# Kernel optimization log

Measured on AMD Instinct MI355X. Metric: run time of the kernel, lower is better.

## Reference

```python
import jax, jax.numpy as jnp
import numpy as np

N_USERS = 20000
N_ITEMS = 30000
N = N_USERS + N_ITEMS          # total nodes
D = 64                          # embedding_dim
EXTRA = 1152                    # 768 metadata + 384 review
E = 500000                      # full-graph edges
NC = 100                        # clusters
HEADS = 2                       # per-layer GATConv heads
CG_HEADS = 4                    # GlobalGATOverClusters hard-codes heads=4
L = 2                           # num_layers
ED = 2                          # edge_dim


def _gat(x, ei, ea, lin, a_src, a_dst, lin_e, a_edge, bias, heads, nnodes):
    """PyG GATConv: add self loops (edge_attr fill='mean'), concat=False -> head mean."""
    C = a_src.shape[-1]
    loop = jnp.arange(nnodes)
    src = jnp.concatenate([ei[0], loop])
    dst = jnp.concatenate([ei[1], loop])
    ea_full = jnp.concatenate([ea, jnp.broadcast_to(ea.mean(0), (nnodes, ea.shape[1]))], 0)
    xh = (x @ lin).reshape(nnodes, heads, C)            # [N,H,C]
    asrc = (xh * a_src).sum(-1)                         # [N,H]
    adst = (xh * a_dst).sum(-1)
    eh = (ea_full @ lin_e).reshape(-1, heads, C)        # [Etot,H,C]
    ae = (eh * a_edge).sum(-1)                          # [Etot,H]
    al = jax.nn.leaky_relu(asrc[src] + adst[dst] + ae, 0.2)
    amax = jax.ops.segment_max(al, dst, num_segments=nnodes)
    ex = jnp.exp(al - amax[dst])
    s = jax.ops.segment_sum(ex, dst, num_segments=nnodes)
    w = ex / (s[dst] + 1e-16)
    out = jax.ops.segment_sum(xh[src] * w[..., None], dst, num_segments=nnodes)
    return out.mean(1) + bias


def _graph_norm(x, weight, bias, mean_scale, eps=1e-5):
    mean = x.mean(0)
    out = x - mean_scale * mean
    var = (out * out).mean(0)
    return weight * out * jax.lax.rsqrt(var + eps) + bias


def _forward(product_extra_features, user_emb, item_emb, fus_w1, fus_b1, fus_w2, fus_b2,
             full_edge_attr, gcn_w, gcn_b,
             cg_lin, cg_att_src, cg_att_dst, cg_lin_edge, cg_att_edge, cg_bias, cluster_edge_attr,
             gat_lin, gat_att_src, gat_att_dst, gat_lin_edge, gat_att_edge, gat_bias,
             gn_weight, gn_bias, gn_mean_scale,
             full_edge_index, cluster_assignment, cluster_edge_index):
    # fusion MLP on item side (dropout is identity at inference)
    h = jnp.maximum(jnp.concatenate([item_emb, product_extra_features], -1) @ fus_w1 + fus_b1, 0.0)
    enriched_items = h @ fus_w2 + fus_b2
    X = jnp.concatenate([user_emb, enriched_items], 0)  # [N, D]

    # per-cluster GCN == one GCN over intra-cluster edges + self loops;
    # nodes in clusters with zero intra edges keep original features
    ei0, ei1 = full_edge_index[0], full_edge_index[1]
    intra = cluster_assignment[ei0] == cluster_assignment[ei1]
    loop = jnp.arange(N)
    row = jnp.concatenate([ei0, loop])
    col = jnp.concatenate([ei1, loop])
    ew = jnp.concatenate([intra.astype(X.dtype), jnp.ones((N,), X.dtype)])
    deg = jax.ops.segment_sum(ew, col, num_segments=N)
    dinv = jnp.where(deg > 0, jax.lax.rsqrt(deg), 0.0)
    norm = dinv[row] * ew * dinv[col]
    xw = X @ gcn_w
    gcn_out = jax.ops.segment_sum(xw[row] * norm[:, None], col, num_segments=N) + gcn_b
    cl_has_edge = jax.ops.segment_sum(intra.astype(jnp.int32), cluster_assignment[ei0], num_segments=NC) > 0
    Xc = jnp.where(cl_has_edge[cluster_assignment][:, None], gcn_out, X)

    # mean pool per cluster
    cnt = jax.ops.segment_sum(jnp.ones((N,), X.dtype), cluster_assignment, num_segments=NC)
    pooled = jax.ops.segment_sum(Xc, cluster_assignment, num_segments=NC) / jnp.maximum(cnt, 1.0)[:, None]

    # global GAT over clusters (inter-cluster multigraph, precomputed)
    cl_upd = _gat(pooled, cluster_edge_index, cluster_edge_attr,
                  cg_lin, cg_att_src, cg_att_dst, cg_lin_edge, cg_att_edge, cg_bias, CG_HEADS, NC)
    Xcomb = Xc + cl_upd[cluster_assignment]

    # full-graph GAT stack with GraphNorm + residual ELU (dropout identity)
    for i in range(L):
        Xin = Xcomb
        g = _gat(Xcomb, full_edge_index, full_edge_attr,
                 gat_lin[i], gat_att_src[i], gat_att_dst[i],
                 gat_lin_edge[i], gat_att_edge[i], gat_bias[i], HEADS, N)
        g = _graph_norm(g, gn_weight[i], gn_bias[i], gn_mean_scale[i])
        Xcomb = jax.nn.elu(g + Xin)

    return Xcomb[:N_USERS], Xcomb[N_USERS:]


def setup_inputs() -> dict:
    rng = np.random.default_rng(0)
    fei = rng.integers(0, N, size=(2, E)).astype(np.int32)
    ca = rng.integers(0, NC, size=(N,)).astype(np.int32)
    fea = rng.random((E, ED)).astype(np.float32)
    # build_cluster_graph: one cluster edge per inter-cluster full edge
    cu, cv = ca[fei[0]], ca[fei[1]]
    m = cu != cv
    cei = np.stack([cu[m], cv[m]]).astype(np.int32)
    cea = fea[m]

    key = jax.random.key(0)
    ks = jax.random.split(key, 24)
    nrm = lambda k, shp, s=0.05: jax.random.normal(k, shp, dtype=jnp.float32) * s
    return {
        'product_extra_features': jax.random.normal(ks[0], (N_ITEMS, EXTRA), dtype=jnp.float32),
        'user_emb': nrm(ks[1], (N_USERS, D), 1.0),
        'item_emb': nrm(ks[2], (N_ITEMS, D), 1.0),
        'fus_w1': nrm(ks[3], (D + EXTRA, 2 * D)),
        'fus_b1': jnp.zeros((2 * D,), jnp.float32),
        'fus_w2': nrm(ks[4], (2 * D, D)),
        'fus_b2': jnp.zeros((D,), jnp.float32),
        'full_edge_attr': jnp.asarray(fea),
        'gcn_w': nrm(ks[5], (D, D)),
        'gcn_b': jnp.zeros((D,), jnp.float32),
        'cg_lin': nrm(ks[6], (D, CG_HEADS * D)),
        'cg_att_src': nrm(ks[7], (CG_HEADS, D)),
        'cg_att_dst': nrm(ks[8], (CG_HEADS, D)),
        'cg_lin_edge': nrm(ks[9], (ED, CG_HEADS * D)),
        'cg_att_edge': nrm(ks[10], (CG_HEADS, D)),
        'cg_bias': jnp.zeros((D,), jnp.float32),
        'cluster_edge_attr': jnp.asarray(cea),
        'gat_lin': nrm(ks[11], (L, D, HEADS * D)),
        'gat_att_src': nrm(ks[12], (L, HEADS, D)),
        'gat_att_dst': nrm(ks[13], (L, HEADS, D)),
        'gat_lin_edge': nrm(ks[14], (L, ED, HEADS * D)),
        'gat_att_edge': nrm(ks[15], (L, HEADS, D)),
        'gat_bias': jnp.zeros((L, D), jnp.float32),
        'gn_weight': jnp.ones((L, D), jnp.float32),
        'gn_bias': jnp.zeros((L, D), jnp.float32),
        'gn_mean_scale': jnp.ones((L, D), jnp.float32),
        'full_edge_index': jnp.asarray(fei),
        'cluster_assignment': jnp.asarray(ca),
        'cluster_edge_index': jnp.asarray(cei),
    }


def reference(product_extra_features, user_emb, item_emb, fus_w1, fus_b1, fus_w2, fus_b2,
              full_edge_attr, gcn_w, gcn_b,
              cg_lin, cg_att_src, cg_att_dst, cg_lin_edge, cg_att_edge, cg_bias, cluster_edge_attr,
              gat_lin, gat_att_src, gat_att_dst, gat_lin_edge, gat_att_edge, gat_bias,
              gn_weight, gn_bias, gn_mean_scale,
              full_edge_index, cluster_assignment, cluster_edge_index):
    return _forward(product_extra_features, user_emb, item_emb, fus_w1, fus_b1, fus_w2, fus_b2,
                    full_edge_attr, gcn_w, gcn_b,
                    cg_lin, cg_att_src, cg_att_dst, cg_lin_edge, cg_att_edge, cg_bias, cluster_edge_attr,
                    gat_lin, gat_att_src, gat_att_dst, gat_lin_edge, gat_att_edge, gat_bias,
                    gn_weight, gn_bias, gn_mean_scale,
                    full_edge_index, cluster_assignment, cluster_edge_index)
```

## Files before the change

### kernel.cpp

```cpp
#include <hip/hip_runtime.h>
#include <hip/hip_bf16.h>

#define N_USERS 20000
#define N_ITEMS 30000
#define NTOT    50000
#define DIM     64
#define EXTRA_D 1152
#define E_EDGES 500000
#define NC      100
#define KTOT    1216
#define KSTEPS  38
#define PPART   16
#define SPART   128

#define B_FEI  1954
#define B_W1   608
#define B_W2   32
#define B_CEI  256
#define PREP_GRID (B_FEI+B_W1+B_W2+B_CEI)

#define FUS_BLKS ((N_ITEMS+127)/128)
#define SCAN1_BLKS ((NTOT+1023)/1024)
#define B_COPY 1250
#define B_CC   64
#define FUS_GRID (FUS_BLKS+SCAN1_BLKS+1+B_COPY+B_CC)

#define SC3_BLKS ((NTOT+255)/256)
#define FILL_BLKS ((E_EDGES+255)/256)
#define DEG_BLKS ((NTOT+3)/4)

typedef __attribute__((ext_vector_type(8))) short short8;
typedef __attribute__((ext_vector_type(4))) float v4f;

__device__ __forceinline__ float wred_sum(float v){
#pragma unroll
  for(int o=32;o;o>>=1) v += __shfl_xor(v,o,64);
  return v;
}
__device__ __forceinline__ int wred_sumi(int v){
#pragma unroll
  for(int o=32;o;o>>=1) v += __shfl_xor(v,o,64);
  return v;
}
__device__ __forceinline__ float lrelu(float x){ return x>0.f? x : 0.2f*x; }
__device__ __forceinline__ short f2bf(float f){
  unsigned u=__float_as_uint(f);
  unsigned r=(u + 0x7FFFu + ((u>>16)&1u))>>16;
  return (short)r;
}
__device__ __forceinline__ unsigned pack_bf2(float x, float y){
  return (unsigned)(unsigned short)f2bf(x) | ((unsigned)(unsigned short)f2bf(y)<<16);
}

__global__ __launch_bounds__(256) void prep_edges_kernel(
    const float* __restrict__ w1, short* __restrict__ w1t,
    const float* __restrict__ w2, short* __restrict__ w2t,
    const int* __restrict__ ca,
    const int* __restrict__ fei, const float* __restrict__ fea,
    int* __restrict__ cnt_dst, int* __restrict__ clflag, int* __restrict__ degI,
    float2* __restrict__ partA,
    const int* __restrict__ cei, const float* __restrict__ cea, int Ec,
    int* __restrict__ ccnt_dst, float2* __restrict__ partB)
{
  __shared__ int hist[NC];
  __shared__ float2 w4[4];
  const int b=blockIdx.x, t=threadIdx.x;
  const int lane=t&63, wv=t>>6;
  if(b < B_FEI){
    int e = b*256+t;
    float a0=0.f,a1=0.f;
    if(e<E_EDGES){
      int s=fei[e], d=fei[E_EDGES+e];
      atomicAdd(&cnt_dst[d],1);
      int cs=ca[s];
      if(cs==ca[d]){ clflag[cs]=1; atomicAdd(&degI[d],1); }
      float2 v=*(const float2*)(fea+2*e);
      a0=v.x; a1=v.y;
    }
    a0=wred_sum(a0); a1=wred_sum(a1);
    if(lane==0) w4[wv]=make_float2(a0,a1);
    __syncthreads();
    if(t==0){ float2 r=w4[0]; for(int i=1;i<4;i++){r.x+=w4[i].x; r.y+=w4[i].y;} partA[b]=r; }
  } else if(b < B_FEI+B_W1){
    int i = (b-B_FEI)*256+t;
    int row = i>>7, n = i&127;
    int s = row>>5, kk = row&31;
    w1t[s*4096 + n*32 + kk] = f2bf(w1[i]);
  } else if(b < B_FEI+B_W1+B_W2){
    int i = (b-B_FEI-B_W1)*256+t;
    int n = i>>6, c = i&63;
    w2t[c*128 + n] = f2bf(w2[i]);
  } else {
    int bb = b-(B_FEI+B_W1+B_W2);
    for(int i=t;i<NC;i+=256) hist[i]=0;
    __syncthreads();
    float a0=0.f,a1=0.f;
    for(int e=bb*256+t; e<Ec; e+=B_CEI*256){
      atomicAdd(&hist[cei[Ec+e]],1);
      float2 v=*(const float2*)(cea+2*e);
      a0+=v.x; a1+=v.y;
    }
    a0=wred_sum(a0); a1=wred_sum(a1);
    if(lane==0) w4[wv]=make_float2(a0,a1);
    __syncthreads();
    if(t==0){ float2 r=w4[0]; for(int i=1;i<4;i++){r.x+=w4[i].x; r.y+=w4[i].y;} partB[bb]=r; }
    for(int i=t;i<NC;i+=256) if(hist[i]) atomicAdd(&ccnt_dst[i],hist[i]);
  }
}

__global__ __launch_bounds__(256) void fus_scan_kernel(
    const float* __restrict__ item, const float* __restrict__ extra,
    const short* __restrict__ w1t, const float* __restrict__ b1,
    const short* __restrict__ w2t, const float* __restrict__ b2,
    float* __restrict__ X,
    const float2* __restrict__ partA, const float2* __restrict__ partB, int Ec,
    const float* __restrict__ cg_le, const float* __restrict__ cg_ae,
    const float* __restrict__ gat_le, const float* __restrict__ gat_ae,
    float* __restrict__ coefs,
    const int* __restrict__ cnt_dst, int* __restrict__ incl, int* __restrict__ bsum,
    const float* __restrict__ u, const int* __restrict__ ca, int* __restrict__ ccnt)
{
  __shared__ short As[128*40];
  __shared__ short Bs[128*40];
  __shared__ short Hs[128*136];
  __shared__ int ssc[256];
  const int tid = threadIdx.x;
  const int b = blockIdx.x;
  if(b < FUS_BLKS){
    const int blk = b;
    const int w = tid>>6, lane = tid&63, quad = lane>>4, l16 = lane&15;
    const int mw = w&1, nw = w>>1;

    v4f acc[4][4];
#pragma unroll
    for(int a=0;a<4;a++)
#pragma unroll
      for(int c=0;c<4;c++) acc[a][c] = (v4f){0.f,0.f,0.f,0.f};

    const int arow = tid>>3;
    const int aoff = (tid&7)*4;
    for(int s=0;s<KSTEPS;s++){
      const int k0 = s*32;
#pragma unroll
      for(int it=0;it<4;it++){
        int r = arow + it*32;
        int col = k0 + aoff;
        int gr = blk*128 + r; if(gr >= N_ITEMS) gr = N_ITEMS-1;
        float4 v = (col < DIM) ? *(const float4*)(item + (size_t)gr*DIM + col)
                               : *(const float4*)(extra + (size_t)gr*EXTRA_D + (col-DIM));
        short4 bv; bv.x=f2bf(v.x); bv.y=f2bf(v.y); bv.z=f2bf(v.z); bv.w=f2bf(v.w);
        *(short4*)&As[r*40 + aoff] = bv;
      }
#pragma unroll
      for(int it=0;it<2;it++){
        int idx = tid + it*256;
        int4 v = *(const int4*)(w1t + (size_t)s*4096 + idx*8);
        int n = idx>>2, kk = (idx&3)*8;
        *(int4*)&Bs[n*40 + kk] = v;
      }
      __syncthreads();
      short8 af[4], bf_[4];
#pragma unroll
      for(int i=0;i<4;i++){
        int m = mw*64 + i*16 + l16;
        af[i]  = *(const short8*)&As[m*40 + quad*8];
        int n = nw*64 + i*16 + l16;
        bf_[i] = *(const short8*)&Bs[n*40 + quad*8];
      }
#pragma unroll
      for(int mi=0;mi<4;mi++)
#pragma unroll
        for(int ni=0;ni<4;ni++)
          acc[mi][ni] = __builtin_amdgcn_mfma_f32_16x16x32_bf16(af[mi], bf_[ni], acc[mi][ni], 0,0,0);
      __syncthreads();
    }

#pragma unroll
    for(int ni=0;ni<4;ni++){
      int n = nw*64 + ni*16 + l16;
      float bias = b1[n];
#pragma unroll
      for(int mi=0;mi<4;mi++){
        int mbase = mw*64 + mi*16 + quad*4;
#pragma unroll
        for(int r=0;r<4;r++){
          float hv = fmaxf(acc[mi][ni][r] + bias, 0.f);
          Hs[(mbase+r)*136 + n] = f2bf(hv);
        }
      }
    }
    __syncthreads();

    v4f acc2[2][4];
#pragma unroll
    for(int a=0;a<2;a++)
#pragma unroll
      for(int c=0;c<4;c++) acc2[a][c] = (v4f){0.f,0.f,0.f,0.f};
#pragma unroll
    for(int ks=0;ks<4;ks++){
      short8 ha[2];
#pragma unroll
      for(int mi=0;mi<2;mi++){
        int m = w*32 + mi*16 + l16;
        ha[mi] = *(const short8*)&Hs[m*136 + ks*32 + quad*8];
      }
#pragma unroll
      for(int ni=0;ni<4;ni++){
        int c = ni*16 + l16;
        short8 wb = *(const short8*)(w2t + c*128 + ks*32 + quad*8);
#pragma unroll
        for(int mi=0;mi<2;mi++)
          acc2[mi][ni] = __builtin_amdgcn_mfma_f32_16x16x32_bf16(ha[mi], wb, acc2[mi][ni], 0,0,0);
      }
    }
#pragma unroll
    for(int ni=0;ni<4;ni++){
      int c = ni*16 + l16;
      float b2v = b2[c];
#pragma unroll
      for(int mi=0;mi<2;mi++){
        int mbase = w*32 + mi*16 + quad*4;
#pragma unroll
        for(int r=0;r<4;r++){
          int row = blk*128 + mbase + r;
          if(row < N_ITEMS) X[(size_t)(N_USERS+row)*64 + c] = acc2[mi][ni][r] + b2v;
        }
      }
    }
  } else if(b < FUS_BLKS+SCAN1_BLKS){
    int sb = b-FUS_BLKS;
    int base = sb*1024 + tid*4;
    int a0=(base  <NTOT)?cnt_dst[base  ]+1:0;
    int a1=(base+1<NTOT)?cnt_dst[base+1]+1:0;
    int a2=(base+2<NTOT)?cnt_dst[base+2]+1:0;
    int a3=(base+3<NTOT)?cnt_dst[base+3]+1:0;
    int l1=a0+a1, l2=l1+a2, l3=l2+a3;
    ssc[tid]=l3; __syncthreads();
    for(int off=1;off<256;off<<=1){
      int v=(tid>=off)?ssc[tid-off]:0; __syncthreads();
      ssc[tid]+=v; __syncthreads();
    }
    int prev = tid? ssc[tid-1]:0;
    if(base  <NTOT) incl[base  ]=prev+a0;
    if(base+1<NTOT) incl[base+1]=prev+l1;
    if(base+2<NTOT) incl[base+2]=prev+l2;
    if(base+3<NTOT) incl[base+3]=prev+l3;
    if(tid==255) bsum[sb]=ssc[255];
  } else if(b == FUS_BLKS+SCAN1_BLKS){
    int lane=tid&63; int wv=tid>>6;
    {
      int hh=wv;
      float v0 = cg_le[hh*64+lane]*cg_ae[hh*64+lane];
      float v1 = cg_le[256 + hh*64+lane]*cg_ae[hh*64+lane];
      v0=wred_sum(v0); v1=wred_sum(v1);
      if(lane==0){ coefs[8+hh]=v0; coefs[12+hh]=v1; }
    }
    {
      int l=wv>>1, hh=wv&1;
      float v0 = gat_le[l*256 + hh*64+lane]     * gat_ae[l*128+hh*64+lane];
      float v1 = gat_le[l*256 + 128 + hh*64+lane]* gat_ae[l*128+hh*64+lane];
      v0=wred_sum(v0); v1=wred_sum(v1);
      if(lane==0){ coefs[16+l*2+hh]=v0; coefs[20+l*2+hh]=v1; }
    }
    __syncthreads();
    if(wv==0){
      float sx=0.f, sy=0.f;
      for(int i=lane;i<B_FEI;i+=64){ float2 v=partA[i]; sx+=v.x; sy+=v.y; }
      sx=wred_sum(sx); sy=wred_sum(sy);
      if(lane==0){ coefs[4]=sx/(float)E_EDGES; coefs[5]=sy/(float)E_EDGES; }
    }
    if(wv==1){
      float sx=0.f, sy=0.f;
      for(int i=lane;i<B_CEI;i+=64){ float2 v=partB[i]; sx+=v.x; sy+=v.y; }
      sx=wred_sum(sx); sy=wred_sum(sy);
      if(lane==0){ coefs[6]=sx/(float)Ec; coefs[7]=sy/(float)Ec; }
    }
  } else if(b < FUS_BLKS+SCAN1_BLKS+1+B_COPY){
    int i = (b-FUS_BLKS-SCAN1_BLKS-1)*256+tid;
    ((float4*)X)[i] = ((const float4*)u)[i];
  } else {
    __shared__ int hist2[NC];
    int bb = b-(FUS_BLKS+SCAN1_BLKS+1+B_COPY);
    for(int i=tid;i<NC;i+=256) hist2[i]=0;
    __syncthreads();
    for(int n=bb*256+tid; n<NTOT; n+=B_CC*256) atomicAdd(&hist2[ca[n]],1);
    __syncthreads();
    for(int i=tid;i<NC;i+=256) if(hist2[i]) atomicAdd(&ccnt[i],hist2[i]);
  }
}

__global__ __launch_bounds__(256) void mid_kernel(
    const int* __restrict__ incl, const int* __restrict__ cnt,
    const int* __restrict__ bsum, int* __restrict__ offs, int* __restrict__ fillptr,
    const float* __restrict__ coefs, int2* __restrict__ slot2,
    const int* __restrict__ degI, float* __restrict__ dinv,
    const int* __restrict__ ccnt_dst, int* __restrict__ coffs, int* __restrict__ cfillp,
    const float* __restrict__ X, const float* __restrict__ gw, float* __restrict__ xw)
{
  __shared__ float Wl[64*64];
  __shared__ float rowb[4][64];
  __shared__ int sprev;
  const int b=blockIdx.x, t=threadIdx.x;
  if(b < SC3_BLKS){
    int blk10 = b>>2;
    if(t<64){
      int v = (t<blk10)? bsum[t] : 0;
      v = wred_sumi(v);
      if(t==0) sprev=v;
    }
    __syncthreads();
    unsigned pk = pack_bf2(coefs[4], coefs[5]);
    int i = b*256+t;
    if(i<NTOT){
      int c=cnt[i];
      int start = sprev + incl[i] - (c+1);
      offs[i]=start; fillptr[i]=start;
      slot2[start+c]=make_int2(i,(int)pk);
      dinv[i]=rsqrtf((float)(degI[i]+1));
    }
    if(i==0) offs[NTOT]=E_EDGES+NTOT;
  } else if(b == SC3_BLKS){
    if(t<64){
      int lane=t;
      int v0 = (2*lane<NC)? ccnt_dst[2*lane]:0;
      int v1 = (2*lane+1<NC)? ccnt_dst[2*lane+1]:0;
      int pair=v0+v1;
      int sc=pair;
#pragma unroll
      for(int o=1;o<64;o<<=1){ int t2=__shfl_up(sc,o,64); if(lane>=o) sc+=t2; }
      int excl = sc - pair;
      if(2*lane<NC){ coffs[2*lane]=excl; cfillp[2*lane]=excl; }
      if(2*lane+1<NC){ coffs[2*lane+1]=excl+v0; cfillp[2*lane+1]=excl+v0; }
      if(lane==63) coffs[NC]=sc;
    }
  } else {
    int bb=b-SC3_BLKS-1;
    const int lane=t&63, wv=t>>6;
    for(int i=t;i<4096;i+=256) Wl[i]=gw[i];
    __syncthreads();
    for(int r=bb*4+wv; r<NTOT; r+=1024*4){
      rowb[wv][lane]=X[(size_t)r*64+lane];
      float acc=0.f;
#pragma unroll 8
      for(int k=0;k<64;k++) acc+=rowb[wv][k]*Wl[k*64+lane];
      xw[(size_t)r*64+lane]=acc;
    }
  }
}

__global__ __launch_bounds__(256) void fill_kernel(
    const int* __restrict__ fei, const float* __restrict__ fea,
    int* __restrict__ fillptr, int2* __restrict__ slot2,
    const int* __restrict__ cei, const float* __restrict__ cea, int Ec,
    int* __restrict__ cfillp, int* __restrict__ cslot_src, float2* __restrict__ cslot_ea)
{
  __shared__ int hist[NC];
  __shared__ int base[NC];
  const int b=blockIdx.x, t=threadIdx.x;
  if(b<FILL_BLKS){
    int e=b*256+t;
    if(e<E_EDGES){
      int dst=fei[E_EDGES+e], src=fei[e];
      int pos=atomicAdd(&fillptr[dst],1);
      float2 v=*(const float2*)(fea+2*e);
      slot2[pos]=make_int2(src,(int)pack_bf2(v.x,v.y));
    }
  } else {
    int bb=b-FILL_BLKS;
    const int chunk=(Ec+127)/128;
    const int beg=bb*chunk;
    const int end=min(beg+chunk,Ec);
    for(int i=t;i<NC;i+=256) hist[i]=0;
    __syncthreads();
    for(int e=beg+t;e<end;e+=256) atomicAdd(&hist[cei[Ec+e]],1);
    __syncthreads();
    for(int i=t;i<NC;i+=256){
      int h=hist[i];
      base[i] = h ? atomicAdd(&cfillp[i],h) : 0;
      hist[i]=0;
    }
    __syncthreads();
    for(int e=beg+t;e<end;e+=256){
      int d=cei[Ec+e];
      int pos = base[d] + atomicAdd(&hist[d],1);
      cslot_src[pos]=cei[e];
      cslot_ea[pos]=make_float2(cea[2*e],cea[2*e+1]);
    }
  }
}

__global__ __launch_bounds__(256) void gcn_agg_kernel(const float* __restrict__ X,
    const float* __restrict__ xw, const float* __restrict__ gcn_b,
    const int* __restrict__ offs, const int2* __restrict__ slot2, const int* __restrict__ ca,
    const float* __restrict__ dinv, const int* __restrict__ flag,
    float* __restrict__ Xc, float* __restrict__ psum){
  __shared__ float2 stg[4][64];
  int lane=threadIdx.x&63, wv=threadIdx.x>>6;
  int n=blockIdx.x*4+wv;
  int beg=offs[n], end=offs[n+1], myca=ca[n];
  float acc=0.f;
  for(int c0=beg;c0<end;c0+=64){
    int j=c0+lane;
    float coef=0.f; int s=0;
    if(j<end){
      s=slot2[j].x;
      if(ca[s]==myca) coef=dinv[s];
    }
    stg[wv][lane]=make_float2(__int_as_float(s),coef);
    unsigned long long bal=__ballot(coef!=0.f);
    while(bal){
      int k=__builtin_ctzll(bal); bal&=bal-1;
      float2 sc=stg[wv][k];
      acc += sc.y * xw[(size_t)__float_as_int(sc.x)*64+lane];
    }
  }
  float gout = dinv[n]*acc + gcn_b[lane];
  float xc = flag[myca] ? gout : X[(size_t)n*64+lane];
  Xc[(size_t)n*64+lane]=xc;
  atomicAdd(&psum[(size_t)(blockIdx.x&(PPART-1))*NC*64 + myca*64+lane], xc);
}

__global__ __launch_bounds__(256) void cluster_prep_kernel(const float* __restrict__ psum,
    const int* __restrict__ ccnt, const float* __restrict__ cg_lin,
    const float* __restrict__ as_, const float* __restrict__ ad_,
    float* __restrict__ xh_c, float* __restrict__ asrc_c, float* __restrict__ adst_c){
  __shared__ float prow[64];
  const int c=blockIdx.x, t=threadIdx.x;
  if(t<64){
    float a=0.f;
#pragma unroll
    for(int p=0;p<PPART;p++) a += psum[(size_t)p*NC*64 + c*64 + t];
    prow[t]=a/fmaxf((float)ccnt[c],1.f);
  }
  __syncthreads();
  float acc=0.f;
#pragma unroll 8
  for(int k=0;k<64;k++) acc += prow[k]*cg_lin[k*256+t];
  xh_c[c*256+t]=acc;
  int lane=t&63, hh=t>>6;
  float s=wred_sum(acc*as_[hh*64+lane]);
  float d=wred_sum(acc*ad_[hh*64+lane]);
  if(lane==0){ asrc_c[c*4+hh]=s; adst_c[c*4+hh]=d; }
}
__global__ __launch_bounds__(256) void cluster_agg_kernel(
    const int* __restrict__ coffs, const int* __restrict__ cslot_src, const float2* __restrict__ cslot_ea,
    const float* __restrict__ asrc_c, const float* __restrict__ adst_c, const float* __restrict__ coefs,
    const float* __restrict__ xh_c, const float* __restrict__ cg_bias, float* __restrict__ cl_upd)
{
  __shared__ float sas[NC*4];
  __shared__ float sW[NC*4];
  __shared__ float ssum[4];
  __shared__ float red[4][64];
  const int c=blockIdx.x, t=threadIdx.x;
  for(int i=t;i<NC*4;i+=256){ sas[i]=asrc_c[i]; sW[i]=0.f; }
  __syncthreads();
  float ad[4], A0[4], A1[4];
#pragma unroll
  for(int h=0;h<4;h++){ ad[h]=adst_c[c*4+h]; A0[h]=coefs[8+h]; A1[h]=coefs[12+h]; }
  const int beg=coffs[c], end=coffs[c+1];
  for(int j=beg+t;j<end;j+=256){
    int s=cslot_src[j]; float2 e=cslot_ea[j];
#pragma unroll
    for(int h=0;h<4;h++){
      float al=lrelu(sas[s*4+h]+ad[h]+e.x*A0[h]+e.y*A1[h]);
      atomicAdd(&sW[s*4+h], __expf(al));
    }
  }
  if(t<4){
    float al=lrelu(sas[c*4+t]+ad[t]+coefs[6]*A0[t]+coefs[7]*A1[t]);
    atomicAdd(&sW[c*4+t], __expf(al));
  }
  __syncthreads();
  const int h=t>>6, lane=t&63;
  float p=0.f;
  if(lane<NC)    p += sW[lane*4+h];
  if(lane+64<NC) p += sW[(lane+64)*4+h];
  p=wred_sum(p);
  if(lane==0) ssum[h]=p+1e-16f;
  __syncthreads();
  float inv=1.f/ssum[h];
  float acc=0.f;
  for(int s=0;s<NC;s++) acc += sW[s*4+h]*xh_c[s*256+h*64+lane];
  red[h][lane]=acc*inv;
  __syncthreads();
  if(t<64) cl_upd[c*64+t]=0.25f*(red[0][t]+red[1][t]+red[2][t]+red[3][t])+cg_bias[t];
}

__global__ __launch_bounds__(256) void gat_xh0_kernel(const float* __restrict__ Xc,
    const float* __restrict__ cl_upd, const int* __restrict__ ca,
    const float* __restrict__ lin, const float* __restrict__ att_s, const float* __restrict__ att_d,
    unsigned* __restrict__ xh2p, float* __restrict__ asrc, float* __restrict__ adst,
    float* __restrict__ Xa){
  __shared__ __align__(16) float Wl[64*128];
  __shared__ float rowb[4][64];
  int t=threadIdx.x;
  for(int i=t;i<8192;i+=256) Wl[i]=lin[i];
  __syncthreads();
  int lane=t&63, wv=t>>6;
  float as0=att_s[lane], as1=att_s[64+lane], ad0=att_d[lane], ad1=att_d[64+lane];
  for(int r=blockIdx.x*4+wv; r<NTOT; r+=gridDim.x*4){
    float xv = Xc[(size_t)r*64+lane] + cl_upd[ca[r]*64+lane];
    Xa[(size_t)r*64+lane]=xv;
    rowb[wv][lane]=xv;
    float x0=0.f,x1=0.f;
#pragma unroll 8
    for(int k=0;k<64;k++){ float q=rowb[wv][k]; x0+=q*Wl[k*128+lane]; x1+=q*Wl[k*128+64+lane]; }
    xh2p[(size_t)r*64+lane]=pack_bf2(x0,x1);
    float p0=wred_sum(x0*as0);
    float p1=wred_sum(x1*as1);
    float q0=wred_sum(x0*ad0);
    float q1=wred_sum(x1*ad1);
    if(lane==0){ asrc[2*r]=p0; asrc[2*r+1]=p1; adst[2*r]=q0; adst[2*r+1]=q1; }
  }
}
__global__ __launch_bounds__(256) void gat_xh1_kernel(const float* __restrict__ g,
    const float* __restrict__ Xres, const float* __restrict__ spart,
    const float* __restrict__ gnw, const float* __restrict__ gnb, const float* __restrict__ gnms,
    const float* __restrict__ lin, const float* __restrict__ att_s, const float* __restrict__ att_d,
    unsigned* __restrict__ xh2p, float* __restrict__ asrc, float* __restrict__ adst,
    float* __restrict__ Xb){
  __shared__ __align__(16) float Wl[64*128];
  __shared__ float rowb[4][64];
  __shared__ float sm[4][64], sv[4][64];
  int t=threadIdx.x;
  int lane=t&63, wv=t>>6;
  for(int i=t;i<8192;i+=256) Wl[i]=lin[i];
  {
    float a0=0.f,a1=0.f;
    for(int p=wv;p<SPART;p+=4){ a0+=spart[p*128+lane]; a1+=spart[p*128+64+lane]; }
    sm[wv][lane]=a0; sv[wv][lane]=a1;
  }
  __syncthreads();
  const float invN = 1.f/(float)NTOT;
  float m=(sm[0][lane]+sm[1][lane]+sm[2][lane]+sm[3][lane])*invN;
  float vsum=(sv[0][lane]+sv[1][lane]+sv[2][lane]+sv[3][lane])*invN;
  float mm=gnms[lane]*m;
  float gwv=rsqrtf(vsum - 2.f*mm*m + mm*mm + 1e-5f)*gnw[lane];
  float gbv=gnb[lane];
  float as0=att_s[lane], as1=att_s[64+lane], ad0=att_d[lane], ad1=att_d[64+lane];
  for(int r=blockIdx.x*4+wv; r<NTOT; r+=gridDim.x*4){
    float z=(g[(size_t)r*64+lane]-mm)*gwv+gbv + Xres[(size_t)r*64+lane];
    float xv = z>0.f? z : __expf(z)-1.f;
    Xb[(size_t)r*64+lane]=xv;
    rowb[wv][lane]=xv;
    float x0=0.f,x1=0.f;
#pragma unroll 8
    for(int k=0;k<64;k++){ float q=rowb[wv][k]; x0+=q*Wl[k*128+lane]; x1+=q*Wl[k*128+64+lane]; }
    xh2p[(size_t)r*64+lane]=pack_bf2(x0,x1);
    float p0=wred_sum(x0*as0);
    float p1=wred_sum(x1*as1);
    float q0=wred_sum(x0*ad0);
    float q1=wred_sum(x1*ad1);
    if(lane==0){ asrc[2*r]=p0; asrc[2*r+1]=p1; adst[2*r]=q0; adst[2*r+1]=q1; }
  }
}

__global__ __launch_bounds__(256) void gat_agg_kernel(const unsigned* __restrict__ xh2p,
    const float2* __restrict__ asrc, const float2* __restrict__ adst,
    const int* __restrict__ offs, const int2* __restrict__ slot2,
    const float* __restrict__ coefs, int layer, const float* __restrict__ bias,
    float* __restrict__ g, float* __restrict__ spart){
  __shared__ float4 stg[4][64];
  __shared__ float s1[64], s2[64];
  int t=threadIdx.x;
  int lane=t&63, wv=t>>6;
  if(t<64){ s1[t]=0.f; s2[t]=0.f; }
  __syncthreads();
  int n=blockIdx.x*4+wv;
  float A00=coefs[16+layer*2+0], A01=coefs[16+layer*2+1];
  float A10=coefs[20+layer*2+0], A11=coefs[20+layer*2+1];
  int beg=offs[n], end=offs[n+1];
  float2 adn=adst[n];
  float s0=0.f,sB=0.f,acc0=0.f,acc1=0.f;
  for(int c0=beg;c0<end;c0+=64){
    int j=c0+lane;
    float ex0=0.f,ex1=0.f; int s=0;
    if(j<end){
      int2 sl=slot2[j];
      s=sl.x;
      unsigned p=(unsigned)sl.y;
      float e0=__uint_as_float(p<<16);
      float e1=__uint_as_float(p&0xffff0000u);
      float2 a=asrc[s];
      ex0=__expf(lrelu(a.x+adn.x+e0*A00+e1*A10));
      ex1=__expf(lrelu(a.y+adn.y+e0*A01+e1*A11));
    }
    s0+=ex0; sB+=ex1;
    stg[wv][lane]=make_float4(__int_as_float(s),ex0,ex1,0.f);
    int cnt=min(64,end-c0);
    int k=0;
    for(; k+4<=cnt; k+=4){
      float4 w0=stg[wv][k], w1=stg[wv][k+1], w2=stg[wv][k+2], w3=stg[wv][k+3];
      unsigned p0=xh2p[(size_t)__float_as_int(w0.x)*64+lane];
      unsigned p1=xh2p[(size_t)__float_as_int(w1.x)*64+lane];
      unsigned p2=xh2p[(size_t)__float_as_int(w2.x)*64+lane];
      unsigned p3=xh2p[(size_t)__float_as_int(w3.x)*64+lane];
      acc0 += w0.y*__uint_as_float(p0<<16) + w1.y*__uint_as_float(p1<<16)
            + w2.y*__uint_as_float(p2<<16) + w3.y*__uint_as_float(p3<<16);
      acc1 += w0.z*__uint_as_float(p0&0xffff0000u) + w1.z*__uint_as_float(p1&0xffff0000u)
            + w2.z*__uint_as_float(p2&0xffff0000u) + w3.z*__uint_as_float(p3&0xffff0000u);
    }
    for(; k<cnt; k++){
      float4 ws=stg[wv][k];
      unsigned pv=xh2p[(size_t)__float_as_int(ws.x)*64+lane];
      acc0 += ws.y*__uint_as_float(pv<<16);
      acc1 += ws.z*__uint_as_float(pv&0xffff0000u);
    }
  }
  s0=wred_sum(s0); sB=wred_sum(sB);
  float gv = 0.5f*(acc0/(s0+1e-16f)+acc1/(sB+1e-16f))+bias[lane];
  g[(size_t)n*64+lane]=gv;
  atomicAdd(&s1[lane],gv);
  atomicAdd(&s2[lane],gv*gv);
  __syncthreads();
  float* dstp = spart + (size_t)(blockIdx.x&(SPART-1))*128;
  if(t<64) atomicAdd(&dstp[t],s1[t]);
  else if(t<128) atomicAdd(&dstp[t],s2[t-64]);
}

__global__ __launch_bounds__(256) void gnorm_elu_kernel(const float* __restrict__ g,
    const float* __restrict__ Xin, const float* __restrict__ spart,
    const float* __restrict__ gw, const float* __restrict__ gb, const float* __restrict__ gms,
    float* __restrict__ outp){
  __shared__ float sst[2][128];
  const float invN = 1.f/(float)NTOT;
  int t=threadIdx.x;
  {
    int d=t&127, hf=t>>7;
    float a=0.f;
    for(int p=hf*64;p<hf*64+64;p++) a+=spart[p*128+d];
    sst[hf][d]=a;
  }
  __syncthreads();
  int i0=blockIdx.x*256+t;
  int d0=(i0&15)*4;
  float mmv[4],gwv[4],gbv[4];
#pragma unroll
  for(int j=0;j<4;j++){
    int d=d0+j;
    float m=(sst[0][d]+sst[1][d])*invN;
    float mm=gms[d]*m;
    mmv[j]=mm;
    gwv[j]=rsqrtf((sst[0][64+d]+sst[1][64+d])*invN-2.f*mm*m+mm*mm+1e-5f)*gw[d];
    gbv[j]=gb[d];
  }
  for(int i=i0;i<NTOT*16;i+=gridDim.x*256){
    float4 gv=((const float4*)g)[i];
    float4 xv=((const float4*)Xin)[i];
    float4 o; float z;
    z=(gv.x-mmv[0])*gwv[0]+gbv[0]+xv.x; o.x = z>0.f? z : __expf(z)-1.f;
    z=(gv.y-mmv[1])*gwv[1]+gbv[1]+xv.y; o.y = z>0.f? z : __expf(z)-1.f;
    z=(gv.z-mmv[2])*gwv[2]+gbv[2]+xv.z; o.z = z>0.f? z : __expf(z)-1.f;
    z=(gv.w-mmv[3])*gwv[3]+gbv[3]+xv.w; o.w = z>0.f? z : __expf(z)-1.f;
    ((float4*)outp)[i]=o;
  }
}

extern "C" void kernel_launch(void* const* d_in, const int* in_sizes, int n_in,
                              void* d_out, int out_size, void* d_ws, size_t ws_size,
                              hipStream_t stream)
{
  const float* extra = (const float*)d_in[0];
  const float* user  = (const float*)d_in[1];
  const float* item  = (const float*)d_in[2];
  const float* fw1 = (const float*)d_in[3];
  const float* fb1 = (const float*)d_in[4];
  const float* fw2 = (const float*)d_in[5];
  const float* fb2 = (const float*)d_in[6];
  const float* fea = (const float*)d_in[7];
  const float* gcn_w = (const float*)d_in[8];
  const float* gcn_b = (const float*)d_in[9];
  const float* cg_lin = (const float*)d_in[10];
  const float* cg_as = (const float*)d_in[11];
  const float* cg_ad = (const float*)d_in[12];
  const float* cg_le = (const float*)d_in[13];
  const float* cg_ae = (const float*)d_in[14];
  const float* cg_bias = (const float*)d_in[15];
  const float* cea = (const float*)d_in[16];
  const float* gat_lin = (const float*)d_in[17];
  const float* gat_as = (const float*)d_in[18];
  const float* gat_ad = (const float*)d_in[19];
  const float* gat_le = (const float*)d_in[20];
  const float* gat_ae = (const float*)d_in[21];
  const float* gat_bias = (const float*)d_in[22];
  const float* gn_w = (const float*)d_in[23];
  const float* gn_b = (const float*)d_in[24];
  const float* gn_ms = (const float*)d_in[25];
  const int* fei = (const int*)d_in[26];
  const int* ca  = (const int*)d_in[27];
  const int* cei = (const int*)d_in[28];
  const int Ec = in_sizes[16]/2;
  float* outp = (float*)d_out;

  char* w = (char*)d_ws;
  auto alloc=[&](size_t b)->char*{ char* p=w; w += (b+255)&~(size_t)255; return p; };

  char* z0 = w;
  int* cnt_dst = (int*)alloc((size_t)NTOT*4);
  int* degI = (int*)alloc((size_t)NTOT*4);
  int* clflag = (int*)alloc(NC*4);
  int* ccnt = (int*)alloc(NC*4);
  int* ccnt_dst = (int*)alloc(NC*4);
  float* psum = (float*)alloc((size_t)PPART*NC*64*4);
  float* spart0 = (float*)alloc((size_t)SPART*128*4);
  float* spart1 = (float*)alloc((size_t)SPART*128*4);
  size_t zbytes = (size_t)(w - z0);

  float2* partA = (float2*)alloc(2048*8);
  float2* partB = (float2*)alloc(256*8);
  float* coefs = (float*)alloc(32*4);
  int* offs = (int*)alloc((size_t)(NTOT+1)*4);
  int* incl = (int*)alloc((size_t)NTOT*4);
  int* bsum = (int*)alloc(64*4);
  int* fillptr = (int*)alloc((size_t)NTOT*4);
  int2* slot2 = (int2*)alloc((size_t)(E_EDGES+NTOT)*8);
  int* coffs = (int*)alloc((size_t)(NC+1)*4);
  int* cfillp = (int*)alloc((size_t)NC*4);
  int* cslot_src = (int*)alloc((size_t)E_EDGES*4);
  float2* cslot_ea = (float2*)alloc((size_t)E_EDGES*8);
  float* dinv = (float*)alloc((size_t)NTOT*4);
  float* xh_c = (float*)alloc(NC*256*4);
  float* asrc_c = (float*)alloc(NC*4*4);
  float* adst_c = (float*)alloc(NC*4*4);
  float* cl_upd = (float*)alloc(NC*64*4);
  float* asrc = (float*)alloc((size_t)NTOT*2*4);
  float* adst = (float*)alloc((size_t)NTOT*2*4);
  short* w1t = (short*)alloc((size_t)KSTEPS*4096*2);
  short* w2t = (short*)alloc((size_t)64*128*2);
  float* bufA = (float*)alloc((size_t)NTOT*64*4);
  float* bufB = (float*)alloc((size_t)NTOT*64*4);
  float* bufC = (float*)alloc((size_t)NTOT*64*4);
  float* bufD = (float*)alloc((size_t)NTOT*64*4);
  unsigned* xh2p = (unsigned*)alloc((size_t)NTOT*64*4);

  float* X  = bufA; float* g  = bufA;
  float* Xc = bufB;
  float* xw = bufC; float* Xb = bufC;
  float* Xa = bufD;

  hipMemsetAsync(z0, 0, zbytes, stream);

  prep_edges_kernel<<<PREP_GRID,256,0,stream>>>(fw1, w1t, fw2, w2t, ca,
                                              fei, fea, cnt_dst, clflag, degI, partA,
                                              cei, cea, Ec, ccnt_dst, partB);
  fus_scan_kernel<<<FUS_GRID,256,0,stream>>>(item, extra, w1t, fb1, w2t, fb2, X,
                                              partA, partB, Ec, cg_le, cg_ae, gat_le, gat_ae, coefs,
                                              cnt_dst, incl, bsum, user, ca, ccnt);
  mid_kernel<<<SC3_BLKS+1+1024,256,0,stream>>>(incl, cnt_dst, bsum, offs, fillptr, coefs, slot2,
                                              degI, dinv, ccnt_dst, coffs, cfillp,
                                              X, gcn_w, xw);
  fill_kernel<<<FILL_BLKS+128,256,0,stream>>>(fei, fea, fillptr, slot2,
                                              cei, cea, Ec, cfillp, cslot_src, cslot_ea);

  gcn_agg_kernel<<<DEG_BLKS,256,0,stream>>>(X, xw, gcn_b, offs, slot2, ca, dinv, clflag, Xc, psum);
  cluster_prep_kernel<<<NC,256,0,stream>>>(psum, ccnt, cg_lin, cg_as, cg_ad, xh_c, asrc_c, adst_c);
  cluster_agg_kernel<<<NC,256,0,stream>>>(coffs, cslot_src, cslot_ea, asrc_c, adst_c, coefs,
                                          xh_c, cg_bias, cl_upd);

  gat_xh0_kernel<<<1024,256,0,stream>>>(Xc, cl_upd, ca, gat_lin, gat_as, gat_ad,
                                        xh2p, asrc, adst, Xa);
  gat_agg_kernel<<<DEG_BLKS,256,0,stream>>>(xh2p, (const float2*)asrc, (const float2*)adst,
                                            offs, slot2, coefs, 0, gat_bias, g, spart0);
  gat_xh1_kernel<<<1024,256,0,stream>>>(g, Xa, spart0, gn_w, gn_b, gn_ms,
                                        gat_lin+64*128, gat_as+128, gat_ad+128,
                                        xh2p, asrc, adst, Xb);
  gat_agg_kernel<<<DEG_BLKS,256,0,stream>>>(xh2p, (const float2*)asrc, (const float2*)adst,
                                            offs, slot2, coefs, 1, gat_bias+64, g, spart1);
  gnorm_elu_kernel<<<512,256,0,stream>>>(g, Xb, spart1, gn_w+64, gn_b+64, gn_ms+64, outp);
}
```

Before: 684.8 us.

## Record edge ranks in prep and fuse CSR fill into mid kernel

The counting pass now stores each edge's atomic rank within its destination bucket, so the fill step can compute slot positions directly from the scan results instead of using a second atomic fillptr pass. This removes the dependency on mid_kernel writing fillptr, which lets mid and fill merge into one launch. The cluster fill likewise recomputes the cluster prefix locally and adds a zero-initialised counter. The cost is an extra 2 MB erank buffer written and read back, plus recomputing the block prefix in every fill block.

Result: faster. 648.2 us (-5.3%).

```diff
diff --git a/kernel.cpp b/kernel.cpp
--- a/kernel.cpp
+++ b/kernel.cpp
@@ -27,6 +27,8 @@
 
 #define SC3_BLKS ((NTOT+255)/256)
 #define FILL_BLKS ((E_EDGES+255)/256)
+#define MF_XW 1024
+#define MF_GRID (SC3_BLKS+1+MF_XW+FILL_BLKS+128)
 #define DEG_BLKS ((NTOT+3)/4)
 
 typedef __attribute__((ext_vector_type(8))) short short8;
@@ -58,7 +60,7 @@
     const int* __restrict__ ca,
     const int* __restrict__ fei, const float* __restrict__ fea,
     int* __restrict__ cnt_dst, int* __restrict__ clflag, int* __restrict__ degI,
-    float2* __restrict__ partA,
+    int* __restrict__ erank, float2* __restrict__ partA,
     const int* __restrict__ cei, const float* __restrict__ cea, int Ec,
     int* __restrict__ ccnt_dst, float2* __restrict__ partB)
 {
@@ -71,7 +73,7 @@
     float a0=0.f,a1=0.f;
     if(e<E_EDGES){
       int s=fei[e], d=fei[E_EDGES+e];
-      atomicAdd(&cnt_dst[d],1);
+      erank[e] = atomicAdd(&cnt_dst[d],1);
       int cs=ca[s];
       if(cs==ca[d]){ clflag[cs]=1; atomicAdd(&degI[d],1); }
       float2 v=*(const float2*)(fea+2*e);
@@ -289,17 +291,24 @@
   }
 }
 
-__global__ __launch_bounds__(256) void mid_kernel(
+__global__ __launch_bounds__(256) void midfill_kernel(
     const int* __restrict__ incl, const int* __restrict__ cnt,
-    const int* __restrict__ bsum, int* __restrict__ offs, int* __restrict__ fillptr,
+    const int* __restrict__ bsum, int* __restrict__ offs,
     const float* __restrict__ coefs, int2* __restrict__ slot2,
     const int* __restrict__ degI, float* __restrict__ dinv,
-    const int* __restrict__ ccnt_dst, int* __restrict__ coffs, int* __restrict__ cfillp,
-    const float* __restrict__ X, const float* __restrict__ gw, float* __restrict__ xw)
+    const int* __restrict__ ccnt_dst, int* __restrict__ coffs,
+    const float* __restrict__ X, const float* __restrict__ gw, float* __restrict__ xw,
+    const int* __restrict__ fei, const float* __restrict__ fea, const int* __restrict__ erank,
+    const int* __restrict__ cei, const float* __restrict__ cea, int Ec,
+    int* __restrict__ cfill0, int* __restrict__ cslot_src, float2* __restrict__ cslot_ea)
 {
   __shared__ float Wl[64*64];
   __shared__ float rowb[4][64];
   __shared__ int sprev;
+  __shared__ int bpref[64];
+  __shared__ int hist[NC];
+  __shared__ int base[NC];
+  __shared__ int clpref[NC];
   const int b=blockIdx.x, t=threadIdx.x;
   if(b < SC3_BLKS){
     int blk10 = b>>2;
@@ -314,7 +323,7 @@
     if(i<NTOT){
       int c=cnt[i];
       int start = sprev + incl[i] - (c+1);
-      offs[i]=start; fillptr[i]=start;
+      offs[i]=start;
       slot2[start+c]=make_int2(i,(int)pk);
       dinv[i]=rsqrtf((float)(degI[i]+1));
     }
@@ -329,44 +338,52 @@
 #pragma unroll
       for(int o=1;o<64;o<<=1){ int t2=__shfl_up(sc,o,64); if(lane>=o) sc+=t2; }
       int excl = sc - pair;
-      if(2*lane<NC){ coffs[2*lane]=excl; cfillp[2*lane]=excl; }
-      if(2*lane+1<NC){ coffs[2*lane+1]=excl+v0; cfillp[2*lane+1]=excl+v0; }
+      if(2*lane<NC) coffs[2*lane]=excl;
+      if(2*lane+1<NC) coffs[2*lane+1]=excl+v0;
       if(lane==63) coffs[NC]=sc;
     }
-  } else {
+  } else if(b < SC3_BLKS+1+MF_XW){
     int bb=b-SC3_BLKS-1;
     const int lane=t&63, wv=t>>6;
     for(int i=t;i<4096;i+=256) Wl[i]=gw[i];
     __syncthreads();
-    for(int r=bb*4+wv; r<NTOT; r+=1024*4){
+    for(int r=bb*4+wv; r<NTOT; r+=MF_XW*4){
       rowb[wv][lane]=X[(size_t)r*64+lane];
       float acc=0.f;
 #pragma unroll 8
       for(int k=0;k<64;k++) acc+=rowb[wv][k]*Wl[k*64+lane];
       xw[(size_t)r*64+lane]=acc;
     }
-  }
-}
-
-__global__ __launch_bounds__(256) void fill_kernel(
-    const int* __restrict__ fei, const float* __restrict__ fea,
-    int* __restrict__ fillptr, int2* __restrict__ slot2,
-    const int* __restrict__ cei, const float* __restrict__ cea, int Ec,
-    int* __restrict__ cfillp, int* __restrict__ cslot_src, float2* __restrict__ cslot_ea)
-{
-  __shared__ int hist[NC];
-  __shared__ int base[NC];
-  const int b=blockIdx.x, t=threadIdx.x;
-  if(b<FILL_BLKS){
-    int e=b*256+t;
+  } else if(b < SC3_BLKS+1+MF_XW+FILL_BLKS){
+    if(t<64){
+      int own = (t<SCAN1_BLKS)? bsum[t]:0;
+      int v=own;
+#pragma unroll
+      for(int o=1;o<64;o<<=1){ int q=__shfl_up(v,o,64); if(t>=o) v+=q; }
+      bpref[t]=v-own;
+    }
+    __syncthreads();
+    int e = (b-(SC3_BLKS+1+MF_XW))*256+t;
     if(e<E_EDGES){
       int dst=fei[E_EDGES+e], src=fei[e];
-      int pos=atomicAdd(&fillptr[dst],1);
+      int start = bpref[dst>>10] + incl[dst] - cnt[dst] - 1;
       float2 v=*(const float2*)(fea+2*e);
-      slot2[pos]=make_int2(src,(int)pack_bf2(v.x,v.y));
+      slot2[start + erank[e]]=make_int2(src,(int)pack_bf2(v.x,v.y));
     }
   } else {
-    int bb=b-FILL_BLKS;
+    if(t<64){
+      int lane=t;
+      int v0 = (2*lane<NC)? ccnt_dst[2*lane]:0;
+      int v1 = (2*lane+1<NC)? ccnt_dst[2*lane+1]:0;
+      int pair=v0+v1;
+      int sc=pair;
+#pragma unroll
+      for(int o=1;o<64;o<<=1){ int t2=__shfl_up(sc,o,64); if(lane>=o) sc+=t2; }
+      int excl = sc - pair;
+      if(2*lane<NC) clpref[2*lane]=excl;
+      if(2*lane+1<NC) clpref[2*lane+1]=excl+v0;
+    }
+    int bb=b-(SC3_BLKS+1+MF_XW+FILL_BLKS);
     const int chunk=(Ec+127)/128;
     const int beg=bb*chunk;
     const int end=min(beg+chunk,Ec);
@@ -376,7 +393,7 @@
     __syncthreads();
     for(int i=t;i<NC;i+=256){
       int h=hist[i];
-      base[i] = h ? atomicAdd(&cfillp[i],h) : 0;
+      base[i] = clpref[i] + (h ? atomicAdd(&cfill0[i],h) : 0);
       hist[i]=0;
     }
     __syncthreads();
@@ -701,6 +718,7 @@
   int* clflag = (int*)alloc(NC*4);
   int* ccnt = (int*)alloc(NC*4);
   int* ccnt_dst = (int*)alloc(NC*4);
+  int* cfill0 = (int*)alloc(NC*4);
   float* psum = (float*)alloc((size_t)PPART*NC*64*4);
   float* spart0 = (float*)alloc((size_t)SPART*128*4);
   float* spart1 = (float*)alloc((size_t)SPART*128*4);
@@ -712,10 +730,9 @@
   int* offs = (int*)alloc((size_t)(NTOT+1)*4);
   int* incl = (int*)alloc((size_t)NTOT*4);
   int* bsum = (int*)alloc(64*4);
-  int* fillptr = (int*)alloc((size_t)NTOT*4);
+  int* erank = (int*)alloc((size_t)E_EDGES*4);
   int2* slot2 = (int2*)alloc((size_t)(E_EDGES+NTOT)*8);
   int* coffs = (int*)alloc((size_t)(NC+1)*4);
-  int* cfillp = (int*)alloc((size_t)NC*4);
   int* cslot_src = (int*)alloc((size_t)E_EDGES*4);
   float2* cslot_ea = (float2*)alloc((size_t)E_EDGES*8);
   float* dinv = (float*)alloc((size_t)NTOT*4);
@@ -741,16 +758,16 @@
   hipMemsetAsync(z0, 0, zbytes, stream);
 
   prep_edges_kernel<<<PREP_GRID,256,0,stream>>>(fw1, w1t, fw2, w2t, ca,
-                                              fei, fea, cnt_dst, clflag, degI, partA,
+                                              fei, fea, cnt_dst, clflag, degI, erank, partA,
                                               cei, cea, Ec, ccnt_dst, partB);
   fus_scan_kernel<<<FUS_GRID,256,0,stream>>>(item, extra, w1t, fb1, w2t, fb2, X,
                                               partA, partB, Ec, cg_le, cg_ae, gat_le, gat_ae, coefs,
                                               cnt_dst, incl, bsum, user, ca, ccnt);
-  mid_kernel<<<SC3_BLKS+1+1024,256,0,stream>>>(incl, cnt_dst, bsum, offs, fillptr, coefs, slot2,
-                                              degI, dinv, ccnt_dst, coffs, cfillp,
-                                              X, gcn_w, xw);
-  fill_kernel<<<FILL_BLKS+128,256,0,stream>>>(fei, fea, fillptr, slot2,
-                                              cei, cea, Ec, cfillp, cslot_src, cslot_ea);
+  midfill_kernel<<<MF_GRID,256,0,stream>>>(incl, cnt_dst, bsum, offs, coefs, slot2,
+                                              degI, dinv, ccnt_dst, coffs,
+                                              X, gcn_w, xw,
+                                              fei, fea, erank,
+                                              cei, cea, Ec, cfill0, cslot_src, cslot_ea);
 
   gcn_agg_kernel<<<DEG_BLKS,256,0,stream>>>(X, xw, gcn_b, offs, slot2, ca, dinv, clflag, Xc, psum);
   cluster_prep_kernel<<<NC,256,0,stream>>>(psum, ccnt, cg_lin, cg_as, cg_ad, xh_c, asrc_c, adst_c);
```
